# Kernel optimization log

Hardware: AMD Instinct MI355X
Metric: run time of the kernel (lower is better)

## Reference

```python
import jax, jax.numpy as jnp
import numpy as np

N = 100000
E = 1600000
IN, HID, OUT = 128, 256, 47


def _glorot(key, shape):
    fan_in, fan_out = shape
    lim = np.sqrt(6.0 / (fan_in + fan_out))
    return jax.random.uniform(key, shape, jnp.float32, -lim, lim)


def setup_inputs() -> dict:
    key = jax.random.key(0)
    ks = jax.random.split(key, 12)
    x = jax.random.normal(ks[0], (N, IN), jnp.float32)
    src = jax.random.randint(ks[1], (E,), 0, N, jnp.int32)
    dst = jax.random.randint(ks[2], (E,), 0, N, jnp.int32)
    dims = [(IN, HID), (HID, HID), (HID, OUT)]
    inp = {"x": x, "src": src, "dst": dst}
    for i, (di, do) in enumerate(dims, 1):
        inp[f"w_self{i}"] = _glorot(ks[2 + 3 * i - 2], (di, do))
        inp[f"w_neigh{i}"] = _glorot(ks[2 + 3 * i - 1], (di, do))
        inp[f"b{i}"] = jnp.zeros((do,), jnp.float32)
    return inp


def sage_conv(x, src, dst, w_self, w_neigh, b):
    n = x.shape[0]
    msg = x[src]                                              # [E, d] gather
    summed = jax.ops.segment_sum(msg, dst, num_segments=n)    # [N, d]
    deg = jax.ops.segment_sum(jnp.ones((src.shape[0],), x.dtype), dst, num_segments=n)
    h_neigh = summed / jnp.maximum(deg, 1.0)[:, None]         # mean aggregate
    return x @ w_self + h_neigh @ w_neigh + b


def reference(x, src, dst, w_self1, w_neigh1, b1, w_self2, w_neigh2, b2, w_self3, w_neigh3, b3):
    h = sage_conv(x, src, dst, w_self1, w_neigh1, b1)
    h = jax.nn.relu(h)  # dropout = identity in eval mode
    h = sage_conv(h, src, dst, w_self2, w_neigh2, b2)
    h = jax.nn.relu(h)
    h = sage_conv(h, src, dst, w_self3, w_neigh3, b3)
    return h
```

## Files before the change

kernel.cpp:

```cpp
#include <hip/hip_runtime.h>

#define N_NODES 100000
#define N_EDGES 1600000

typedef __attribute__((ext_vector_type(8))) _Float16 half8;
typedef __attribute__((ext_vector_type(4))) _Float16 half4v;
typedef __attribute__((ext_vector_type(4))) float floatx4;


__global__ void deg_rank(const int* __restrict__ dst, int* __restrict__ deg,
                         int* __restrict__ rank, int e) {
    int i = blockIdx.x * blockDim.x + threadIdx.x;
    if (i < e) rank[i] = atomicAdd(&deg[dst[i]], 1);
}

__global__ __launch_bounds__(256) void scan_partial(const int* __restrict__ deg,
                                                    int* __restrict__ bsum, int n) {
    __shared__ int wsum[4];
    int t = threadIdx.x;
    int base = blockIdx.x * 2048 + t * 8;
    int tsum = 0;
    #pragma unroll
    for (int k = 0; k < 8; ++k) {
        int idx = base + k;
        tsum += (idx < n) ? deg[idx] : 0;
    }
    #pragma unroll
    for (int d = 1; d < 64; d <<= 1) tsum += __shfl_xor(tsum, d, 64);
    if ((t & 63) == 0) wsum[t >> 6] = tsum;
    __syncthreads();
    if (t == 0) bsum[blockIdx.x] = wsum[0] + wsum[1] + wsum[2] + wsum[3];
}

__global__ void scan_blocksums(const int* __restrict__ bsum, int* __restrict__ bbase, int nb) {
    int t = threadIdx.x;
    int v = (t < nb) ? bsum[t] : 0;
    int s = v;
    #pragma unroll
    for (int d = 1; d < 64; d <<= 1) {
        int u = __shfl_up(s, d, 64);
        if (t >= d) s += u;
    }
    if (t < nb) bbase[t] = s - v;
    if (t == 63) bbase[nb] = s;
}

__global__ __launch_bounds__(256) void scan_write(const int* __restrict__ deg,
                                                  const int* __restrict__ bbase,
                                                  int* __restrict__ offs, int n, int nb) {
    __shared__ int wsum[4];
    int t = threadIdx.x;
    int lane = t & 63, w = t >> 6;
    int base = blockIdx.x * 2048 + t * 8;
    int v[8];
    #pragma unroll
    for (int k = 0; k < 8; ++k) {
        int idx = base + k;
        v[k] = (idx < n) ? deg[idx] : 0;
    }
    int tsum = 0;
    #pragma unroll
    for (int k = 0; k < 8; ++k) { int x = v[k]; v[k] = tsum; tsum += x; }
    int s = tsum;
    #pragma unroll
    for (int d = 1; d < 64; d <<= 1) {
        int u = __shfl_up(s, d, 64);
        if (lane >= d) s += u;
    }
    if (lane == 63) wsum[w] = s;
    __syncthreads();
    int wb = 0;
    for (int j = 0; j < w; ++j) wb += wsum[j];
    int texcl = bbase[blockIdx.x] + wb + (s - tsum);
    #pragma unroll
    for (int k = 0; k < 8; ++k) {
        int idx = base + k;
        if (idx < n) offs[idx] = texcl + v[k];
    }
    if (blockIdx.x == 0 && t == 0) offs[n] = bbase[nb];
}

__global__ void fill_csr2(const int* __restrict__ src, const int* __restrict__ dst,
                          const int* __restrict__ offs, const int* __restrict__ rank,
                          int* __restrict__ csr, int e) {
    int i = blockIdx.x * blockDim.x + threadIdx.x;
    if (i < e) csr[offs[dst[i]] + rank[i]] = src[i];
}


__global__ void cvt_f16(const float4* __restrict__ in, half4v* __restrict__ oh, int n4) {
    int i = blockIdx.x * blockDim.x + threadIdx.x;
    if (i >= n4) return;
    float4 v = in[i];
    half4v h;
    h[0] = (_Float16)v.x; h[1] = (_Float16)v.y;
    h[2] = (_Float16)v.z; h[3] = (_Float16)v.w;
    oh[i] = h;
}


__global__ void prep_all(const float* __restrict__ ws1, const float* __restrict__ wn1,
                         const float* __restrict__ ws2, const float* __restrict__ wn2,
                         const float* __restrict__ ws3, const float* __restrict__ wn3,
                         _Float16* __restrict__ o1s, _Float16* __restrict__ o1n,
                         _Float16* __restrict__ o2s, _Float16* __restrict__ o2n,
                         _Float16* __restrict__ o3c) {
    int i = blockIdx.x * blockDim.x + threadIdx.x;
    if (i < 65536) {
        const float* W = (i < 32768) ? ws1 : wn1;
        _Float16* O = (i < 32768) ? o1s : o1n;
        int j = i & 32767;
        int nn = j >> 7, k = j & 127;
        O[j] = (_Float16)W[k * 256 + nn];
    } else if (i < 196608) {
        int j = i - 65536;
        const float* W = (j < 65536) ? ws2 : wn2;
        _Float16* O = (j < 65536) ? o2s : o2n;
        j &= 65535;
        int nn = j >> 8, k = j & 255;
        O[j] = (_Float16)W[k * 256 + nn];
    } else if (i < 221184) {
        int j = i - 196608;
        const float* W = (j < 12288) ? ws3 : wn3;
        _Float16* O = o3c + ((j < 12288) ? 0 : 12288);
        j = (j < 12288) ? j : j - 12288;
        int nn = j >> 8, k = j & 255;
        O[j] = (nn < 47) ? (_Float16)W[k * 47 + nn] : (_Float16)0.f;
    }
}


__global__ __launch_bounds__(256) void aggP(const _Float16* __restrict__ Xp,
                                            const int* __restrict__ csr,
                                            const int* __restrict__ offs,
                                            _Float16* __restrict__ Pp, int n) {
    int node = blockIdx.x * 4 + (threadIdx.x >> 6);
    int lane = threadIdx.x & 63;
    int qtr = lane >> 4;
    int sl = lane & 15;
    if (node >= n) return;
    int e0 = offs[node], e1 = offs[node + 1];
    float a[8] = {0.f, 0.f, 0.f, 0.f, 0.f, 0.f, 0.f, 0.f};
    int e = e0;
    for (; e + 16 <= e1; e += 16) {
        int s0 = csr[e + qtr];
        int s1 = csr[e + 4 + qtr];
        int s2 = csr[e + 8 + qtr];
        int s3 = csr[e + 12 + qtr];
        half8 u0 = ((const half8*)(Xp + (size_t)s0 * 128))[sl];
        half8 u1 = ((const half8*)(Xp + (size_t)s1 * 128))[sl];
        half8 u2 = ((const half8*)(Xp + (size_t)s2 * 128))[sl];
        half8 u3 = ((const half8*)(Xp + (size_t)s3 * 128))[sl];
        #pragma unroll
        for (int j = 0; j < 8; ++j) a[j] += (float)u0[j];
        #pragma unroll
        for (int j = 0; j < 8; ++j) a[j] += (float)u1[j];
        #pragma unroll
        for (int j = 0; j < 8; ++j) a[j] += (float)u2[j];
        #pragma unroll
        for (int j = 0; j < 8; ++j) a[j] += (float)u3[j];
    }
    for (; e + 8 <= e1; e += 8) {
        int s0 = csr[e + qtr];
        int s1 = csr[e + 4 + qtr];
        half8 u0 = ((const half8*)(Xp + (size_t)s0 * 128))[sl];
        half8 u1 = ((const half8*)(Xp + (size_t)s1 * 128))[sl];
        #pragma unroll
        for (int j = 0; j < 8; ++j) a[j] += (float)u0[j];
        #pragma unroll
        for (int j = 0; j < 8; ++j) a[j] += (float)u1[j];
    }
    for (; e + 4 <= e1; e += 4) {
        int s = csr[e + qtr];
        half8 u = ((const half8*)(Xp + (size_t)s * 128))[sl];
        #pragma unroll
        for (int j = 0; j < 8; ++j) a[j] += (float)u[j];
    }
    int rem = e1 - e;
    if (qtr < rem) {
        int s = csr[e + qtr];
        half8 u = ((const half8*)(Xp + (size_t)s * 128))[sl];
        #pragma unroll
        for (int j = 0; j < 8; ++j) a[j] += (float)u[j];
    }
    #pragma unroll
    for (int j = 0; j < 8; ++j) {
        a[j] += __shfl_xor(a[j], 16);
        a[j] += __shfl_xor(a[j], 32);
    }
    if (lane < 16) {
        float inv = 1.0f / fmaxf((float)(e1 - e0), 1.0f);
        half8 rh;
        #pragma unroll
        for (int j = 0; j < 8; ++j) rh[j] = (_Float16)(a[j] * inv);
        ((half8*)(Pp + (size_t)node * 128))[sl] = rh;
    }
}

__global__ __launch_bounds__(256) void agg_l3(const _Float16* __restrict__ Y,
                                              const float* __restrict__ S,
                                              const int* __restrict__ csr,
                                              const int* __restrict__ offs,
                                              float* __restrict__ out, int n) {
    int node = blockIdx.x * 4 + (threadIdx.x >> 6);
    int lane = threadIdx.x & 63;
    int qtr = lane >> 4;
    int sl = lane & 15;
    int c = sl < 12 ? sl : 11;
    if (node >= n) return;
    int e0 = offs[node], e1 = offs[node + 1];
    float a0 = 0.f, a1 = 0.f, a2 = 0.f, a3 = 0.f;
    int e = e0;
    for (; e + 8 <= e1; e += 8) {
        int s0 = csr[e + qtr];
        int s1 = csr[e + 4 + qtr];
        half4v f0 = ((const half4v*)(Y + (size_t)s0 * 48))[c];
        half4v f1 = ((const half4v*)(Y + (size_t)s1 * 48))[c];
        a0 += (float)f0[0] + (float)f1[0];
        a1 += (float)f0[1] + (float)f1[1];
        a2 += (float)f0[2] + (float)f1[2];
        a3 += (float)f0[3] + (float)f1[3];
    }
    for (; e + 4 <= e1; e += 4) {
        int s = csr[e + qtr];
        half4v f = ((const half4v*)(Y + (size_t)s * 48))[c];
        a0 += (float)f[0]; a1 += (float)f[1]; a2 += (float)f[2]; a3 += (float)f[3];
    }
    int rem = e1 - e;
    if (qtr < rem) {
        int s = csr[e + qtr];
        half4v f = ((const half4v*)(Y + (size_t)s * 48))[c];
        a0 += (float)f[0]; a1 += (float)f[1]; a2 += (float)f[2]; a3 += (float)f[3];
    }
    a0 += __shfl_xor(a0, 16); a0 += __shfl_xor(a0, 32);
    a1 += __shfl_xor(a1, 16); a1 += __shfl_xor(a1, 32);
    a2 += __shfl_xor(a2, 16); a2 += __shfl_xor(a2, 32);
    a3 += __shfl_xor(a3, 16); a3 += __shfl_xor(a3, 32);
    if (lane < 12) {
        float inv = 1.0f / fmaxf((float)(e1 - e0), 1.0f);
        float4 sv = ((const float4*)(S + (size_t)node * 48))[c];
        float r[4] = {sv.x + a0 * inv, sv.y + a1 * inv, sv.z + a2 * inv, sv.w + a3 * inv};
        #pragma unroll
        for (int k = 0; k < 4; ++k) {
            int col = c * 4 + k;
            if (col < 47) out[(size_t)node * 47 + col] = r[k];
        }
    }
}


template <int NTILES, int OUTFMT>
__global__ __launch_bounds__(256, 3) void gemm64(
    const _Float16* __restrict__ A1h, const _Float16* __restrict__ A2h,
    const _Float16* __restrict__ W1, const _Float16* __restrict__ W2,
    const float* __restrict__ bias, float* __restrict__ outS, _Float16* __restrict__ outY,
    _Float16* __restrict__ outh, int n, int K, int relu, int phases) {
    constexpr int NPAD = NTILES * 16;
    constexpr int LDT = 36;
    __shared__ _Float16 Bs[2][NPAD * LDT];

    const int t = threadIdx.x;
    const int bm = blockIdx.x * 64;
    const int colbase = blockIdx.y * NPAD;
    const int lane = t & 63;
    const int w = t >> 6;
    const int quad = lane >> 4;
    const int tl = lane & 15;
    const int r0 = bm + w * 16 + tl;
    const size_t PS = (size_t)n * 128;

    floatx4 acc[NTILES];
    #pragma unroll
    for (int j = 0; j < NTILES; ++j) acc[j] = (floatx4){0.f, 0.f, 0.f, 0.f};

    const int spp = K >> 5;
    const int nsteps = phases * spp;

    const int tr = t >> 1;
    const int koff = (t & 1) * 16;
    const bool stager = (t < 2 * NPAD);

    half8 pb0, pb1;
    half8 aA = {0}, aB = {0};

    auto wload = [&](int s2) {
        int ph2 = (s2 >= spp) ? 1 : 0;
        int k02 = (ph2 ? s2 - spp : s2) << 5;
        const _Float16* W = ph2 ? W2 : W1;
        const half8* p = (const half8*)(W + (size_t)(colbase + tr) * K + k02 + koff);
        pb0 = p[0]; pb1 = p[1];
    };
    auto aload = [&](int s2, half8& d) {
        int ph2 = (s2 >= spp) ? 1 : 0;
        int k02 = (ph2 ? s2 - spp : s2) << 5;
        const _Float16* Ah = ph2 ? A2h : A1h;
        int kq = k02 + quad * 8;
        const _Float16* Ab = Ah + ((kq >> 7) ? PS : (size_t)0) + (kq & 127);
        d = (half8){0};
        if (r0 < n) d = *(const half8*)(Ab + (size_t)r0 * 128);
    };

    if (stager) {
        wload(0);
        *(half8*)&Bs[0][tr * LDT + koff]     = pb0;
        *(half8*)&Bs[0][tr * LDT + koff + 8] = pb1;
        wload(1);
    }
    aload(0, aA);
    aload(1, aB);
    __syncthreads();

    for (int s = 0; s < nsteps; s += 2) {
        {
            if (s + 1 < nsteps && stager) {
                *(half8*)&Bs[1][tr * LDT + koff]     = pb0;
                *(half8*)&Bs[1][tr * LDT + koff + 8] = pb1;
                if (s + 2 < nsteps) wload(s + 2);
            }
            half8 ca = aA;
            if (s + 2 < nsteps) aload(s + 2, aA);
            #pragma unroll
            for (int nt = 0; nt < NTILES; ++nt) {
                half8 bh = *(const half8*)&Bs[0][(nt * 16 + tl) * LDT + quad * 8];
                acc[nt] = __builtin_amdgcn_mfma_f32_16x16x32_f16(ca, bh, acc[nt], 0, 0, 0);
            }
            asm volatile("s_waitcnt lgkmcnt(0)" ::: "memory");
            __builtin_amdgcn_sched_barrier(0);
            __builtin_amdgcn_s_barrier();
        }
        {
            int s1 = s + 1;
            if (s1 + 1 < nsteps && stager) {
                *(half8*)&Bs[0][tr * LDT + koff]     = pb0;
                *(half8*)&Bs[0][tr * LDT + koff + 8] = pb1;
                if (s1 + 2 < nsteps) wload(s1 + 2);
            }
            half8 ca = aB;
            if (s1 + 2 < nsteps) aload(s1 + 2, aB);
            #pragma unroll
            for (int nt = 0; nt < NTILES; ++nt) {
                half8 bh = *(const half8*)&Bs[1][(nt * 16 + tl) * LDT + quad * 8];
                acc[nt] = __builtin_amdgcn_mfma_f32_16x16x32_f16(ca, bh, acc[nt], 0, 0, 0);
            }
            asm volatile("s_waitcnt lgkmcnt(0)" ::: "memory");
            __builtin_amdgcn_sched_barrier(0);
            __builtin_amdgcn_s_barrier();
        }
    }

    #pragma unroll
    for (int nt = 0; nt < NTILES; ++nt) {
        int gc = colbase + nt * 16 + tl;
        #pragma unroll
        for (int r = 0; r < 4; ++r) {
            int gr = bm + w * 16 + quad * 4 + r;
            if (gr >= n) continue;
            float v = acc[nt][r];
            if (OUTFMT == 1) {
                v += bias[gc];
                if (relu) v = fmaxf(v, 0.f);
                outh[(size_t)(gc >> 7) * PS + (size_t)gr * 128 + (gc & 127)] = (_Float16)v;
            } else {
                if (gc < 48) {
                    v += (gc < 47) ? bias[gc] : 0.f;
                    outS[(size_t)gr * 48 + gc] = v;
                } else {
                    outY[(size_t)gr * 48 + (gc - 48)] = (_Float16)v;
                }
            }
        }
    }
}


template <int NTILES, int OUTFMT>
__global__ __launch_bounds__(256, 2) void gemm_mfma(
    const _Float16* __restrict__ A1h, const _Float16* __restrict__ A2h,
    const _Float16* __restrict__ W1, const _Float16* __restrict__ W2,
    const float* __restrict__ bias, float* __restrict__ outS, _Float16* __restrict__ outY,
    _Float16* __restrict__ outh, int n, int K, int dout, int relu, int phases) {
    constexpr int NPAD = NTILES * 16;
    constexpr int LDT = 36;
    __shared__ _Float16 Bs[2][NPAD * LDT];

    const int t = threadIdx.x;
    const int bm = blockIdx.x * 128;
    const int lane = t & 63;
    const int w = t >> 6;
    const int quad = lane >> 4;
    const int tl = lane & 15;
    const int r0 = bm + w * 32 + tl;
    const int r1 = r0 + 16;
    const size_t PS = (size_t)n * 128;

    floatx4 acc[2][NTILES];
    #pragma unroll
    for (int i = 0; i < 2; ++i)
        #pragma unroll
        for (int j = 0; j < NTILES; ++j) acc[i][j] = (floatx4){0.f, 0.f, 0.f, 0.f};

    const int spp = K >> 5;
    const int nsteps = phases * spp;

    half8 pb0, pb1, pb2, pb3;
    half8 a0A = {0}, a1A = {0}, a0B = {0}, a1B = {0};

    auto wload = [&](int s2) {
        int ph2 = (s2 >= spp) ? 1 : 0;
        int k02 = (ph2 ? s2 - spp : s2) << 5;
        const _Float16* W = ph2 ? W2 : W1;
        const half8* p = (const half8*)(W + (size_t)t * K + k02);
        pb0 = p[0]; pb1 = p[1]; pb2 = p[2]; pb3 = p[3];
    };
    auto aload = [&](int s2, half8& d0, half8& d1) {
        int ph2 = (s2 >= spp) ? 1 : 0;
        int k02 = (ph2 ? s2 - spp : s2) << 5;
        const _Float16* Ah = ph2 ? A2h : A1h;
        int kq = k02 + quad * 8;
        const _Float16* Ab = Ah + ((kq >> 7) ? PS : (size_t)0) + (kq & 127);
        d0 = (half8){0}; d1 = (half8){0};
        if (r0 < n) d0 = *(const half8*)(Ab + (size_t)r0 * 128);
        if (r1 < n) d1 = *(const half8*)(Ab + (size_t)r1 * 128);
    };

    if (t < NPAD) {
        wload(0);
        *(half8*)&Bs[0][t * LDT + 0]  = pb0;
        *(half8*)&Bs[0][t * LDT + 8]  = pb1;
        *(half8*)&Bs[0][t * LDT + 16] = pb2;
        *(half8*)&Bs[0][t * LDT + 24] = pb3;
        wload(1);
    }
    aload(0, a0A, a1A);
    aload(1, a0B, a1B);
    __syncthreads();

    for (int s = 0; s < nsteps; s += 2) {
        {
            if (s + 1 < nsteps && t < NPAD) {
                *(half8*)&Bs[1][t * LDT + 0]  = pb0;
                *(half8*)&Bs[1][t * LDT + 8]  = pb1;
                *(half8*)&Bs[1][t * LDT + 16] = pb2;
                *(half8*)&Bs[1][t * LDT + 24] = pb3;
                if (s + 2 < nsteps) wload(s + 2);
            }
            half8 ca0 = a0A, ca1 = a1A;
            if (s + 2 < nsteps) aload(s + 2, a0A, a1A);
            #pragma unroll
            for (int nt = 0; nt < NTILES; ++nt) {
                half8 bh = *(const half8*)&Bs[0][(nt * 16 + tl) * LDT + quad * 8];
                acc[0][nt] = __builtin_amdgcn_mfma_f32_16x16x32_f16(ca0, bh, acc[0][nt], 0, 0, 0);
                acc[1][nt] = __builtin_amdgcn_mfma_f32_16x16x32_f16(ca1, bh, acc[1][nt], 0, 0, 0);
            }
            asm volatile("s_waitcnt lgkmcnt(0)" ::: "memory");
            __builtin_amdgcn_sched_barrier(0);
            __builtin_amdgcn_s_barrier();
        }
        {
            int s1 = s + 1;
            if (s1 + 1 < nsteps && t < NPAD) {
                *(half8*)&Bs[0][t * LDT + 0]  = pb0;
                *(half8*)&Bs[0][t * LDT + 8]  = pb1;
                *(half8*)&Bs[0][t * LDT + 16] = pb2;
                *(half8*)&Bs[0][t * LDT + 24] = pb3;
                if (s1 + 2 < nsteps) wload(s1 + 2);
            }
            half8 ca0 = a0B, ca1 = a1B;
            if (s1 + 2 < nsteps) aload(s1 + 2, a0B, a1B);
            #pragma unroll
            for (int nt = 0; nt < NTILES; ++nt) {
                half8 bh = *(const half8*)&Bs[1][(nt * 16 + tl) * LDT + quad * 8];
                acc[0][nt] = __builtin_amdgcn_mfma_f32_16x16x32_f16(ca0, bh, acc[0][nt], 0, 0, 0);
                acc[1][nt] = __builtin_amdgcn_mfma_f32_16x16x32_f16(ca1, bh, acc[1][nt], 0, 0, 0);
            }
            asm volatile("s_waitcnt lgkmcnt(0)" ::: "memory");
            __builtin_amdgcn_sched_barrier(0);
            __builtin_amdgcn_s_barrier();
        }
    }

    #pragma unroll
    for (int mt = 0; mt < 2; ++mt) {
        #pragma unroll
        for (int nt = 0; nt < NTILES; ++nt) {
            int gc = nt * 16 + tl;
            if (OUTFMT == 1 && gc >= dout) continue;
            #pragma unroll
            for (int r = 0; r < 4; ++r) {
                int gr = bm + w * 32 + mt * 16 + quad * 4 + r;
                if (gr >= n) continue;
                float v = acc[mt][nt][r];
                if (OUTFMT == 1) {
                    v += bias[gc];
                    if (relu) v = fmaxf(v, 0.f);
                    outh[(size_t)(gc >> 7) * PS + (size_t)gr * 128 + (gc & 127)] = (_Float16)v;
                } else {
                    if (gc < 48) {
                        v += (gc < 47) ? bias[gc] : 0.f;
                        outS[(size_t)gr * 48 + gc] = v;
                    } else {
                        outY[(size_t)gr * 48 + (gc - 48)] = (_Float16)v;
                    }
                }
            }
        }
    }
}

extern "C" void kernel_launch(void* const* d_in, const int* in_sizes, int n_in,
                              void* d_out, int out_size, void* d_ws, size_t ws_size,
                              hipStream_t stream) {
    (void)in_sizes; (void)n_in; (void)out_size;
    const int N = N_NODES, E = N_EDGES;
    const float* x = (const float*)d_in[0];
    const int* src = (const int*)d_in[1];
    const int* dst = (const int*)d_in[2];
    const float* w_self1 = (const float*)d_in[3];
    const float* w_neigh1 = (const float*)d_in[4];
    const float* b1 = (const float*)d_in[5];
    const float* w_self2 = (const float*)d_in[6];
    const float* w_neigh2 = (const float*)d_in[7];
    const float* b2 = (const float*)d_in[8];
    const float* w_self3 = (const float*)d_in[9];
    const float* w_neigh3 = (const float*)d_in[10];
    const float* b3 = (const float*)d_in[11];
    float* out = (float*)d_out;

    _Float16* Ph = (_Float16*)d_ws;
    _Float16* Hh = Ph + (size_t)N * 256;
    int* deg = (int*)(Hh + (size_t)N * 256);
    int* offs = deg + N;
    int* csr = offs + N + 4;
    _Float16* wbuf = (_Float16*)(csr + E);
    _Float16* w1s = wbuf;
    _Float16* w1n = w1s + 32768;
    _Float16* w2s = w1n + 32768;
    _Float16* w2n = w2s + 65536;
    _Float16* w3c = w2n + 65536;
    int* bsum = (int*)(w3c + 24576);
    int* bbase = bsum + 64;
    int* rank = (int*)Ph;
    _Float16* xh = Ph + (size_t)N * 128;
    float* S = (float*)Ph;
    _Float16* Y = (_Float16*)(S + (size_t)N * 48);
    size_t used = (size_t)((char*)(bbase + 64) - (char*)d_ws);
    used = (used + 255) & ~(size_t)255;
    _Float16* H2 = (_Float16*)((char*)d_ws + used);
    const bool dbuf = (used + (size_t)N * 256 * sizeof(_Float16)) <= ws_size;

    const int NB = (N + 2047) / 2048;

    hipMemsetAsync(deg, 0, N * sizeof(int), stream);
    deg_rank<<<(E + 255) / 256, 256, 0, stream>>>(dst, deg, rank, E);
    scan_partial<<<NB, 256, 0, stream>>>(deg, bsum, N);
    scan_blocksums<<<1, 64, 0, stream>>>(bsum, bbase, NB);
    scan_write<<<NB, 256, 0, stream>>>(deg, bbase, offs, N, NB);
    fill_csr2<<<(E + 255) / 256, 256, 0, stream>>>(src, dst, offs, rank, csr, E);

    cvt_f16<<<(N * 128 / 4 + 255) / 256, 256, 0, stream>>>((const float4*)x, (half4v*)xh,
                                                           N * 128 / 4);
    prep_all<<<(221184 + 255) / 256, 256, 0, stream>>>(w_self1, w_neigh1, w_self2, w_neigh2,
                                                       w_self3, w_neigh3, w1s, w1n, w2s, w2n,
                                                       w3c);

    const int g64 = (N + 63) / 64;
    int aggGrid = (N + 3) / 4;

    aggP<<<aggGrid, 256, 0, stream>>>(xh, csr, offs, Ph, N);
    gemm64<8, 1><<<dim3(g64, 2), 256, 0, stream>>>(xh, Ph, w1s, w1n, b1, nullptr, nullptr,
                                                   Hh, N, 128, 1, 2);
    aggP<<<aggGrid, 256, 0, stream>>>(Hh, csr, offs, Ph, N);
    aggP<<<aggGrid, 256, 0, stream>>>(Hh + (size_t)N * 128, csr, offs, Ph + (size_t)N * 128, N);
    const _Float16* Hcur;
    if (dbuf) {
        gemm64<8, 1><<<dim3(g64, 2), 256, 0, stream>>>(Hh, Ph, w2s, w2n, b2, nullptr, nullptr,
                                                       H2, N, 256, 1, 2);
        Hcur = H2;
    } else {
        gemm_mfma<16, 1><<<(N + 127) / 128, 256, 0, stream>>>(Hh, Ph, w2s, w2n, b2, nullptr,
                                                              nullptr, Hh, N, 256, 256, 1, 2);
        Hcur = Hh;
    }
    gemm64<6, 2><<<dim3(g64, 1), 256, 0, stream>>>(Hcur, nullptr, w3c, nullptr, b3, S, Y,
                                                   nullptr, N, 256, 0, 1);
    agg_l3<<<aggGrid, 256, 0, stream>>>(Y, S, csr, offs, out, N);
}
```

Measured before the change: 601.0 us.

## Preload all A fragments into registers and template GEMM loop bounds

The GEMM kernel now takes K, steps-per-phase and phase count as template parameters, so the k-loop is fully unrolled. All A-operand fragments for the block are loaded into registers up front instead of being double-buffered two steps ahead, which exposes every global load at once for maximum memory-level parallelism. Weight staging is simplified so each of the first NPAD threads loads a full 32-element row slice per step. This raises register pressure (up to 16 half8 A registers with launch bounds of 3 blocks/CU) and could force spills or lower occupancy.

```diff
diff --git a/kernel.cpp b/kernel.cpp
--- a/kernel.cpp
+++ b/kernel.cpp
@@ -249,14 +249,16 @@
 }
 
 
-template <int NTILES, int OUTFMT>
-__global__ __launch_bounds__(256, 3) void gemm64(
+template <int NTILES, int OUTFMT, int SPP, int PHASES>
+__global__ __launch_bounds__(256, 3) void gemm64r(
     const _Float16* __restrict__ A1h, const _Float16* __restrict__ A2h,
     const _Float16* __restrict__ W1, const _Float16* __restrict__ W2,
     const float* __restrict__ bias, float* __restrict__ outS, _Float16* __restrict__ outY,
-    _Float16* __restrict__ outh, int n, int K, int relu, int phases) {
+    _Float16* __restrict__ outh, int n, int relu) {
     constexpr int NPAD = NTILES * 16;
     constexpr int LDT = 36;
+    constexpr int NSTEPS = SPP * PHASES;
+    constexpr int K = SPP * 32;
     __shared__ _Float16 Bs[2][NPAD * LDT];
 
     const int t = threadIdx.x;
@@ -273,79 +275,58 @@
     #pragma unroll
     for (int j = 0; j < NTILES; ++j) acc[j] = (floatx4){0.f, 0.f, 0.f, 0.f};
 
-    const int spp = K >> 5;
-    const int nsteps = phases * spp;
-
-    const int tr = t >> 1;
-    const int koff = (t & 1) * 16;
-    const bool stager = (t < 2 * NPAD);
-
-    half8 pb0, pb1;
-    half8 aA = {0}, aB = {0};
-
+    half8 areg[NSTEPS];
+    #pragma unroll
+    for (int ph = 0; ph < PHASES; ++ph) {
+        const _Float16* Ah = (ph == 0) ? A1h : A2h;
+        #pragma unroll
+        for (int st = 0; st < SPP; ++st) {
+            int kq = st * 32 + quad * 8;
+            const _Float16* Ab = Ah + ((kq >> 7) ? PS : (size_t)0) + (kq & 127);
+            half8 d = (half8){0};
+            if (r0 < n) d = *(const half8*)(Ab + (size_t)r0 * 128);
+            areg[ph * SPP + st] = d;
+        }
+    }
+
+    half8 pb0, pb1, pb2, pb3;
     auto wload = [&](int s2) {
-        int ph2 = (s2 >= spp) ? 1 : 0;
-        int k02 = (ph2 ? s2 - spp : s2) << 5;
+        int ph2 = (s2 >= SPP) ? 1 : 0;
+        int k02 = (ph2 ? s2 - SPP : s2) * 32;
         const _Float16* W = ph2 ? W2 : W1;
-        const half8* p = (const half8*)(W + (size_t)(colbase + tr) * K + k02 + koff);
-        pb0 = p[0]; pb1 = p[1];
+        const half8* p = (const half8*)(W + (size_t)(colbase + t) * K + k02);
+        pb0 = p[0]; pb1 = p[1]; pb2 = p[2]; pb3 = p[3];
     };
-    auto aload = [&](int s2, half8& d) {
-        int ph2 = (s2 >= spp) ? 1 : 0;
-        int k02 = (ph2 ? s2 - spp : s2) << 5;
-        const _Float16* Ah = ph2 ? A2h : A1h;
-        int kq = k02 + quad * 8;
-        const _Float16* Ab = Ah + ((kq >> 7) ? PS : (size_t)0) + (kq & 127);
-        d = (half8){0};
-        if (r0 < n) d = *(const half8*)(Ab + (size_t)r0 * 128);
-    };
-
-    if (stager) {
+
+    if (t < NPAD) {
         wload(0);
-        *(half8*)&Bs[0][tr * LDT + koff]     = pb0;
-        *(half8*)&Bs[0][tr * LDT + koff + 8] = pb1;
-        wload(1);
-    }
-    aload(0, aA);
-    aload(1, aB);
+        *(half8*)&Bs[0][t * LDT + 0]  = pb0;
+        *(half8*)&Bs[0][t * LDT + 8]  = pb1;
+        *(half8*)&Bs[0][t * LDT + 16] = pb2;
+        *(half8*)&Bs[0][t * LDT + 24] = pb3;
+        if (NSTEPS > 1) wload(1);
+    }
     __syncthreads();
 
-    for (int s = 0; s < nsteps; s += 2) {
-        {
-            if (s + 1 < nsteps && stager) {
-                *(half8*)&Bs[1][tr * LDT + koff]     = pb0;
-                *(half8*)&Bs[1][tr * LDT + koff + 8] = pb1;
-                if (s + 2 < nsteps) wload(s + 2);
-            }
-            half8 ca = aA;
-            if (s + 2 < nsteps) aload(s + 2, aA);
-            #pragma unroll
-            for (int nt = 0; nt < NTILES; ++nt) {
-                half8 bh = *(const half8*)&Bs[0][(nt * 16 + tl) * LDT + quad * 8];
-                acc[nt] = __builtin_amdgcn_mfma_f32_16x16x32_f16(ca, bh, acc[nt], 0, 0, 0);
-            }
-            asm volatile("s_waitcnt lgkmcnt(0)" ::: "memory");
-            __builtin_amdgcn_sched_barrier(0);
-            __builtin_amdgcn_s_barrier();
-        }
-        {
-            int s1 = s + 1;
-            if (s1 + 1 < nsteps && stager) {
-                *(half8*)&Bs[0][tr * LDT + koff]     = pb0;
-                *(half8*)&Bs[0][tr * LDT + koff + 8] = pb1;
-                if (s1 + 2 < nsteps) wload(s1 + 2);
-            }
-            half8 ca = aB;
-            if (s1 + 2 < nsteps) aload(s1 + 2, aB);
-            #pragma unroll
-            for (int nt = 0; nt < NTILES; ++nt) {
-                half8 bh = *(const half8*)&Bs[1][(nt * 16 + tl) * LDT + quad * 8];
-                acc[nt] = __builtin_amdgcn_mfma_f32_16x16x32_f16(ca, bh, acc[nt], 0, 0, 0);
-            }
-            asm volatile("s_waitcnt lgkmcnt(0)" ::: "memory");
-            __builtin_amdgcn_sched_barrier(0);
-            __builtin_amdgcn_s_barrier();
-        }
+    #pragma unroll
+    for (int s = 0; s < NSTEPS; ++s) {
+        const int cur = s & 1;
+        if (s + 1 < NSTEPS && t < NPAD) {
+            *(half8*)&Bs[cur ^ 1][t * LDT + 0]  = pb0;
+            *(half8*)&Bs[cur ^ 1][t * LDT + 8]  = pb1;
+            *(half8*)&Bs[cur ^ 1][t * LDT + 16] = pb2;
+            *(half8*)&Bs[cur ^ 1][t * LDT + 24] = pb3;
+            if (s + 2 < NSTEPS) wload(s + 2);
+        }
+        half8 ca = areg[s];
+        #pragma unroll
+        for (int nt = 0; nt < NTILES; ++nt) {
+            half8 bh = *(const half8*)&Bs[cur][(nt * 16 + tl) * LDT + quad * 8];
+            acc[nt] = __builtin_amdgcn_mfma_f32_16x16x32_f16(ca, bh, acc[nt], 0, 0, 0);
+        }
+        asm volatile("s_waitcnt lgkmcnt(0)" ::: "memory");
+        __builtin_amdgcn_sched_barrier(0);
+        __builtin_amdgcn_s_barrier();
     }
 
     #pragma unroll
@@ -567,21 +548,21 @@
     int aggGrid = (N + 3) / 4;
 
     aggP<<<aggGrid, 256, 0, stream>>>(xh, csr, offs, Ph, N);
-    gemm64<8, 1><<<dim3(g64, 2), 256, 0, stream>>>(xh, Ph, w1s, w1n, b1, nullptr, nullptr,
-                                                   Hh, N, 128, 1, 2);
+    gemm64r<8, 1, 4, 2><<<dim3(g64, 2), 256, 0, stream>>>(xh, Ph, w1s, w1n, b1, nullptr,
+                                                          nullptr, Hh, N, 1);
     aggP<<<aggGrid, 256, 0, stream>>>(Hh, csr, offs, Ph, N);
     aggP<<<aggGrid, 256, 0, stream>>>(Hh + (size_t)N * 128, csr, offs, Ph + (size_t)N * 128, N);
     const _Float16* Hcur;
     if (dbuf) {
-        gemm64<8, 1><<<dim3(g64, 2), 256, 0, stream>>>(Hh, Ph, w2s, w2n, b2, nullptr, nullptr,
-                                                       H2, N, 256, 1, 2);
+        gemm64r<8, 1, 8, 2><<<dim3(g64, 2), 256, 0, stream>>>(Hh, Ph, w2s, w2n, b2, nullptr,
+                                                              nullptr, H2, N, 1);
         Hcur = H2;
     } else {
         gemm_mfma<16, 1><<<(N + 127) / 128, 256, 0, stream>>>(Hh, Ph, w2s, w2n, b2, nullptr,
                                                               nullptr, Hh, N, 256, 256, 1, 2);
         Hcur = Hh;
     }
-    gemm64<6, 2><<<dim3(g64, 1), 256, 0, stream>>>(Hcur, nullptr, w3c, nullptr, b3, S, Y,
-                                                   nullptr, N, 256, 0, 1);
+    gemm64r<6, 2, 8, 1><<<dim3(g64, 1), 256, 0, stream>>>(Hcur, nullptr, w3c, nullptr, b3,
+                                                          S, Y, nullptr, N, 0);
     agg_l3<<<aggGrid, 256, 0, stream>>>(Y, S, csr, offs, out, N);
 }
```

New measurement: 636.4 us. +5.9%, slower.
